# Kernel optimization log

Hardware: AMD Instinct MI355X
Metric: run time of the kernel (lower is better)

## Reference

```python
import jax, jax.numpy as jnp
import numpy as np

N, E, IN_DIM, OUT_DIM, R = 50000, 800000, 128, 128, 8


def setup_inputs() -> dict:
    key = jax.random.key(0)
    k1, k2, k3, k4, k5 = jax.random.split(key, 5)
    x = jax.random.normal(k1, (N, IN_DIM), dtype=jnp.float32)
    edge_index = jax.random.randint(k2, (2, E), 0, N, dtype=jnp.int32)
    edge_type = jax.random.randint(k3, (E,), 0, R, dtype=jnp.int32)
    # Xavier-uniform-ish init for parameters
    lim_w = float(np.sqrt(6.0 / (IN_DIM + OUT_DIM)))
    weight = jax.random.uniform(k4, (R, IN_DIM, OUT_DIM), dtype=jnp.float32, minval=-lim_w, maxval=lim_w)
    self_weight = jax.random.uniform(k5, (IN_DIM, OUT_DIM), dtype=jnp.float32, minval=-lim_w, maxval=lim_w)
    return {"x": x, "weight": weight, "self_weight": self_weight,
            "edge_index": edge_index, "edge_type": edge_type}


def reference(x, weight, self_weight, edge_index, edge_type):
    n = x.shape[0]
    r = weight.shape[0]
    d_out = weight.shape[2]
    src, dst = edge_index[0], edge_index[1]
    # undirected: symmetrize edges (directed=False)
    src_all = jnp.concatenate([src, dst])          # [2E]
    dst_all = jnp.concatenate([dst, src])          # [2E]
    et_all = jnp.concatenate([edge_type, edge_type])  # [2E]
    # transform all nodes by every relation weight once: [R, N, D_out]
    xw = jnp.einsum('ni,rio->rno', x, weight)
    # gather per-edge messages already transformed by their relation's W_r
    msg = xw[et_all, src_all]                      # [2E, D_out]
    # fused (relation, dst) segment id -> per-relation scatter-add
    seg = et_all.astype(jnp.int32) * n + dst_all
    agg = jax.ops.segment_sum(msg, seg, num_segments=r * n).reshape(r, n, d_out)
    deg = jax.ops.segment_sum(jnp.ones_like(seg, dtype=x.dtype), seg,
                              num_segments=r * n).reshape(r, n)
    deg_inv = jnp.where(deg > 0, 1.0 / jnp.maximum(deg, 1.0), jnp.zeros_like(deg))
    out = jnp.sum(agg * deg_inv[..., None], axis=0)  # [N, D_out]
    out = out + x @ self_weight                       # self-loop
    return out
```

## Files before the change

kernel.cpp:

```cpp
#include <hip/hip_runtime.h>

#define NN 50000
#define EE 800000
#define RR 8
#define DD 128
#define SS (NN*RR)
#define TE (2*EE)
#define NB 782
#define NBLK 391
#define NS (NB*NBLK)

typedef __attribute__((ext_vector_type(8))) short bf16x8;
typedef __attribute__((ext_vector_type(4))) float f32x4;

__device__ __forceinline__ unsigned short f2bf(float f){
  unsigned int u = __float_as_uint(f);
  u += 0x7fffu + ((u >> 16) & 1u);
  return (unsigned short)(u >> 16);
}
__device__ __forceinline__ float bf_lo(unsigned int w){ return __uint_as_float(w << 16); }
__device__ __forceinline__ float bf_hi(unsigned int w){ return __uint_as_float(w & 0xffff0000u); }

__device__ __forceinline__ void acc8(float* a, uint4 u){
  a[0] += bf_lo(u.x); a[1] += bf_hi(u.x);
  a[2] += bf_lo(u.y); a[3] += bf_hi(u.y);
  a[4] += bf_lo(u.z); a[5] += bf_hi(u.z);
  a[6] += bf_lo(u.w); a[7] += bf_hi(u.w);
}
__device__ __forceinline__ unsigned int pack2(float a, float b){
  return ((unsigned int)f2bf(b) << 16) | (unsigned int)f2bf(a);
}

__device__ __forceinline__ void dir_edge(const int* ei, const int* et, int j,
                                         int& s, int& d, int& t){
  if (j < EE){ s = ei[j]; d = ei[EE + j]; t = et[j]; }
  else { int jj = j - EE; s = ei[EE + jj]; d = ei[jj]; t = et[jj]; }
}

__global__ __launch_bounds__(256) void k_hist(const int* __restrict__ ei,
                                              const int* __restrict__ et,
                                              int* __restrict__ hist){
  __shared__ int h[NB];
  int tid = threadIdx.x, bid = blockIdx.x;
  for (int i = tid; i < NB; i += 256) h[i] = 0;
  __syncthreads();
  int j0 = bid*4096;
  for (int k = tid; k < 4096; k += 256){
    int j = j0 + k;
    if (j < TE){
      int s, d, t; dir_edge(ei, et, j, s, d, t);
      atomicAdd(&h[d >> 6], 1);
    }
  }
  __syncthreads();
  for (int i = tid; i < NB; i += 256) hist[i*NBLK + bid] = h[i];
}

__global__ __launch_bounds__(256) void k_scan1(int* __restrict__ hist,
                                               int* __restrict__ blksum){
  __shared__ int sd[256];
  int b = blockIdx.x, tid = threadIdx.x;
  int base = b*1024 + tid*4;
  int v0 = (base+0 < NS) ? hist[base+0] : 0;
  int v1 = (base+1 < NS) ? hist[base+1] : 0;
  int v2 = (base+2 < NS) ? hist[base+2] : 0;
  int v3 = (base+3 < NS) ? hist[base+3] : 0;
  int ts = v0+v1+v2+v3;
  sd[tid] = ts; __syncthreads();
  for (int o = 1; o < 256; o <<= 1){
    int t = (tid >= o) ? sd[tid-o] : 0;
    __syncthreads();
    sd[tid] += t;
    __syncthreads();
  }
  int ex = sd[tid] - ts;
  if (base+0 < NS) hist[base+0] = ex; ex += v0;
  if (base+1 < NS) hist[base+1] = ex; ex += v1;
  if (base+2 < NS) hist[base+2] = ex; ex += v2;
  if (base+3 < NS) hist[base+3] = ex;
  if (tid == 255) blksum[b] = sd[255];
}

__global__ __launch_bounds__(512) void k_scan2(int* __restrict__ blksum, int nb){
  __shared__ int sd[512];
  int tid = threadIdx.x;
  int v = (tid < nb) ? blksum[tid] : 0;
  sd[tid] = v; __syncthreads();
  for (int o = 1; o < 512; o <<= 1){
    int t = (tid >= o) ? sd[tid-o] : 0;
    __syncthreads();
    sd[tid] += t;
    __syncthreads();
  }
  if (tid < nb) blksum[tid] = sd[tid] - v;
}

__global__ __launch_bounds__(256) void k_scan3(int* __restrict__ hist,
                                               const int* __restrict__ blksum){
  int i = blockIdx.x*blockDim.x + threadIdx.x;
  if (i < NS) hist[i] += blksum[i >> 10];
}

__global__ __launch_bounds__(256) void k_part(const int* __restrict__ ei,
                                              const int* __restrict__ et,
                                              const int* __restrict__ S,
                                              unsigned int* __restrict__ P){
  __shared__ int cur[NB];
  int tid = threadIdx.x, bid = blockIdx.x;
  for (int i = tid; i < NB; i += 256) cur[i] = S[i*NBLK + bid];
  __syncthreads();
  int j0 = bid*4096;
  for (int k = tid; k < 4096; k += 256){
    int j = j0 + k;
    if (j < TE){
      int s, d, t; dir_edge(ei, et, j, s, d, t);
      int b = d >> 6;
      int p = atomicAdd(&cur[b], 1);
      P[p] = (unsigned int)s | ((unsigned int)(d & 63) << 17)
           | ((unsigned int)t << 23);
    }
  }
}

__global__ __launch_bounds__(256) void k_build(const unsigned int* __restrict__ P,
                                               const int* __restrict__ S,
                                               int* __restrict__ esrc,
                                               int* __restrict__ offs){
  __shared__ int h[512], cu[512], sd[256];
  int tid = threadIdx.x, b = blockIdx.x;
  int pstart = S[b*NBLK];
  int pend   = (b+1 < NB) ? S[(b+1)*NBLK] : TE;
  int ne = pend - pstart;
  h[2*tid] = 0; h[2*tid+1] = 0;
  __syncthreads();
  for (int k = tid; k < ne; k += 256){
    unsigned int u = P[pstart + k];
    int lseg = (int)(((u >> 17) & 63u)*8u + (u >> 23));
    atomicAdd(&h[lseg], 1);
  }
  __syncthreads();
  int v0 = h[2*tid], v1 = h[2*tid+1];
  int ts = v0 + v1;
  sd[tid] = ts; __syncthreads();
  for (int o = 1; o < 256; o <<= 1){
    int t = (tid >= o) ? sd[tid-o] : 0;
    __syncthreads();
    sd[tid] += t;
    __syncthreads();
  }
  int ex = sd[tid] - ts;
  cu[2*tid]   = pstart + ex;
  cu[2*tid+1] = pstart + ex + v0;
  int seg0 = b*512;
  if (seg0 + 2*tid     < SS) offs[seg0 + 2*tid]     = cu[2*tid];
  if (seg0 + 2*tid + 1 < SS) offs[seg0 + 2*tid + 1] = cu[2*tid+1];
  if (b == NB-1 && tid == 0) offs[SS] = TE;
  __syncthreads();
  for (int k = tid; k < ne; k += 256){
    unsigned int u = P[pstart + k];
    int lseg = (int)(((u >> 17) & 63u)*8u + (u >> 23));
    int r = atomicAdd(&cu[lseg], 1);
    esrc[r] = (int)(u & 0x1ffffu);
  }
}

__global__ __launch_bounds__(256) void k_conv(const float* __restrict__ x,
                                              const float* __restrict__ w,
                                              const float* __restrict__ sw,
                                              unsigned short* __restrict__ xb,
                                              unsigned short* __restrict__ wb){
  int i = blockIdx.x*blockDim.x + threadIdx.x;
  const int M1 = NN*DD/4;
  if (i < M1){
    float4 v = ((const float4*)x)[i];
    ushort4 o;
    o.x = f2bf(v.x); o.y = f2bf(v.y); o.z = f2bf(v.z); o.w = f2bf(v.w);
    ((ushort4*)xb)[i] = o;
  } else {
    int j = i - M1;
    if (j < 9*DD*DD){
      int r = j >> 14; int rem = j & 16383; int n = rem >> 7; int k = rem & 127;
      float v = (r < 8) ? w[r*16384 + k*128 + n] : sw[k*128 + n];
      wb[j] = f2bf(v);
    }
  }
}

__device__ __forceinline__ void issue4(const unsigned short* __restrict__ xb,
                                       int idxw, int gb, int gl,
                                       int ebase, int n, uint4 (&u)[4]){
  #pragma unroll
  for (int e = 0; e < 4; ++e){
    u[e] = make_uint4(0u,0u,0u,0u);
    if (e < n){
      int s = __shfl(idxw, gb + ebase + e);
      u[e] = *(const uint4*)(xb + (size_t)s*DD + gl*8);
    }
  }
}

__global__ __launch_bounds__(256, 2) void k_fused(
    const unsigned short* __restrict__ xb,
    const unsigned short* __restrict__ wb,
    const int* __restrict__ offs,
    const int* __restrict__ esrc,
    float* __restrict__ out)
{
  __shared__ __align__(16) unsigned short A[32][1160];
  const int tid  = threadIdx.x;
  const int wave = tid >> 6, lane = tid & 63;
  const int l15  = lane & 15, quad = lane >> 4;
  const int gw   = quad;
  const int gl   = l15;
  const int gb   = gw << 4;
  const int rowbase = blockIdx.x * 32;
  const int rw0 = rowbase + 8*wave;

  #pragma unroll
  for (int p = 0; p < 2; ++p){
    int rowl = 8*wave + 2*gw + p;
    int gd = rowbase + rowl;
    uint4 u = make_uint4(0u,0u,0u,0u);
    if (gd < NN) u = *(const uint4*)(xb + (size_t)gd*DD + gl*8);
    *(uint4*)&A[rowl][8*128 + gl*8] = u;
  }

  int oidx = rw0*8 + lane;
  int c0i = (oidx     < SS) ? oidx     : SS;
  int c1i = (oidx + 1 < SS) ? oidx + 1 : SS;
  int voff = offs[c0i];
  int vend = offs[c1i];
  int vcnt = vend - voff;

  int idxv[16];
  #pragma unroll
  for (int i = 0; i < 16; ++i){
    int off = __shfl(voff, gb + i);
    int cnt = __shfl(vcnt, gb + i);
    idxv[i] = (gl < cnt) ? esrc[off + gl] : 0;
  }

  uint4 U0[2][4], U1[2][4];
  {
    int c0 = __shfl(vcnt, gb + 0); c0 = c0 < 4 ? c0 : 4;
    int c1 = __shfl(vcnt, gb + 1); c1 = c1 < 4 ? c1 : 4;
    issue4(xb, idxv[0], gb, gl, 0, c0, U0[0]);
    issue4(xb, idxv[1], gb, gl, 0, c1, U1[0]);
  }

  #pragma unroll
  for (int ii = 0; ii < 16; ii += 2){
    const int cur = (ii >> 1) & 1;
    const int nxt = cur ^ 1;
    if (ii + 2 < 16){
      int c0 = __shfl(vcnt, gb + ii + 2); c0 = c0 < 4 ? c0 : 4;
      int c1 = __shfl(vcnt, gb + ii + 3); c1 = c1 < 4 ? c1 : 4;
      issue4(xb, idxv[ii+2], gb, gl, 0, c0, U0[nxt]);
      issue4(xb, idxv[ii+3], gb, gl, 0, c1, U1[nxt]);
    }
    int cnt0 = __shfl(vcnt, gb + ii),     cnt1 = __shfl(vcnt, gb + ii + 1);
    int off0 = __shfl(voff, gb + ii),     off1 = __shfl(voff, gb + ii + 1);
    int cm0  = cnt0 < 16 ? cnt0 : 16,     cm1  = cnt1 < 16 ? cnt1 : 16;
    float a0[8] = {0.f,0.f,0.f,0.f,0.f,0.f,0.f,0.f};
    float a1[8] = {0.f,0.f,0.f,0.f,0.f,0.f,0.f,0.f};
    #pragma unroll
    for (int e = 0; e < 4; ++e){ acc8(a0, U0[cur][e]); acc8(a1, U1[cur][e]); }
    int e0 = cm0 < 4 ? cm0 : 4, e1 = cm1 < 4 ? cm1 : 4;
    while (e0 < cm0 || e1 < cm1){
      int n0 = cm0 - e0; n0 = n0 < 0 ? 0 : (n0 > 4 ? 4 : n0);
      int n1 = cm1 - e1; n1 = n1 < 0 ? 0 : (n1 > 4 ? 4 : n1);
      uint4 t0[4], t1[4];
      issue4(xb, idxv[ii],   gb, gl, e0, n0, t0);
      issue4(xb, idxv[ii+1], gb, gl, e1, n1, t1);
      #pragma unroll
      for (int e = 0; e < 4; ++e){ acc8(a0, t0[e]); acc8(a1, t1[e]); }
      e0 += n0; e1 += n1;
    }
    if (cnt0 > 16){
      for (int e2 = 16; e2 < cnt0; ++e2){
        int s = esrc[off0 + e2];
        uint4 u = *(const uint4*)(xb + (size_t)s*DD + gl*8);
        acc8(a0, u);
      }
    }
    if (cnt1 > 16){
      for (int e2 = 16; e2 < cnt1; ++e2){
        int s = esrc[off1 + e2];
        uint4 u = *(const uint4*)(xb + (size_t)s*DD + gl*8);
        acc8(a1, u);
      }
    }
    float s0 = cnt0 > 0 ? 1.0f/(float)cnt0 : 0.f;
    float s1 = cnt1 > 0 ? 1.0f/(float)cnt1 : 0.f;
    int rowl = 8*wave + 2*gw + (ii >> 3);
    uint4 w0, w1;
    w0.x = pack2(a0[0]*s0, a0[1]*s0);
    w0.y = pack2(a0[2]*s0, a0[3]*s0);
    w0.z = pack2(a0[4]*s0, a0[5]*s0);
    w0.w = pack2(a0[6]*s0, a0[7]*s0);
    w1.x = pack2(a1[0]*s1, a1[1]*s1);
    w1.y = pack2(a1[2]*s1, a1[3]*s1);
    w1.z = pack2(a1[4]*s1, a1[5]*s1);
    w1.w = pack2(a1[6]*s1, a1[7]*s1);
    *(uint4*)&A[rowl][((ii    ) & 7)*128 + gl*8] = w0;
    *(uint4*)&A[rowl][((ii + 1) & 7)*128 + gl*8] = w1;
  }

  __syncthreads();

  f32x4 C[2][2];
  #pragma unroll
  for (int m = 0; m < 2; ++m){ C[m][0] = (f32x4)(0.f); C[m][1] = (f32x4)(0.f); }

  #pragma unroll
  for (int rr = 0; rr < 9; ++rr){
    const unsigned short* wr = wb + rr * 16384;
    bf16x8 bfrag[2][4];
    #pragma unroll
    for (int nt = 0; nt < 2; ++nt)
      #pragma unroll
      for (int ks = 0; ks < 4; ++ks)
        bfrag[nt][ks] = *(const bf16x8*)(wr + (wave*32 + nt*16 + l15)*128 + ks*32 + quad*8);
    #pragma unroll
    for (int m = 0; m < 2; ++m){
      #pragma unroll
      for (int ks = 0; ks < 4; ++ks){
        bf16x8 af = *(const bf16x8*)&A[m*16 + l15][rr*128 + ks*32 + quad*8];
        C[m][0] = __builtin_amdgcn_mfma_f32_16x16x32_bf16(af, bfrag[0][ks], C[m][0], 0, 0, 0);
        C[m][1] = __builtin_amdgcn_mfma_f32_16x16x32_bf16(af, bfrag[1][ks], C[m][1], 0, 0, 0);
      }
    }
  }

  #pragma unroll
  for (int m = 0; m < 2; ++m){
    #pragma unroll
    for (int nt = 0; nt < 2; ++nt){
      #pragma unroll
      for (int i = 0; i < 4; ++i){
        int row = m*16 + quad*4 + i;
        int gd  = rowbase + row;
        int col = wave*32 + nt*16 + l15;
        if (gd < NN) out[gd*DD + col] = C[m][nt][i];
      }
    }
  }
}

extern "C" void kernel_launch(void* const* d_in, const int* in_sizes, int n_in,
                              void* d_out, int out_size, void* d_ws, size_t ws_size,
                              hipStream_t stream){
  const float* x  = (const float*)d_in[0];
  const float* w  = (const float*)d_in[1];
  const float* sw = (const float*)d_in[2];
  const int*   ei = (const int*)d_in[3];
  const int*   et = (const int*)d_in[4];
  float* out = (float*)d_out;
  char* ws = (char*)d_ws;

  if (ws_size < (size_t)21100000) return;

  unsigned short* xb = (unsigned short*)(ws + 0);
  int*          hist = (int*)(ws + 0);
  int*        blksum = (int*)(ws + 1223168);
  unsigned int*    P = (unsigned int*)(ws + 1225216);
  int*          esrc = (int*)(ws + 12800000);
  int*          offs = (int*)(ws + 19200000);
  unsigned short* wb = (unsigned short*)(ws + 20800016);

  k_hist <<<NBLK, 256, 0, stream>>>(ei, et, hist);
  k_scan1<<<(NS + 1023)/1024, 256, 0, stream>>>(hist, blksum);
  k_scan2<<<1, 512, 0, stream>>>(blksum, (NS + 1023)/1024);
  k_scan3<<<(NS + 255)/256, 256, 0, stream>>>(hist, blksum);
  k_part <<<NBLK, 256, 0, stream>>>(ei, et, hist, P);
  k_build<<<NB, 256, 0, stream>>>(P, hist, esrc, offs);
  k_conv <<<(NN*DD/4 + 9*DD*DD + 255)/256, 256, 0, stream>>>(x, w, sw, xb, wb);
  k_fused<<<(NN + 31)/32, 256, 0, stream>>>(xb, wb, offs, esrc, out);
}
```

Measured before the change: 279.5 us.

## Shrink fused tile to 16 rows per block for higher occupancy

Each fused block now handles 16 destination nodes instead of 32. Each 16-lane group aggregates one node's 8 relation segments rather than two nodes' worth, so LDS per block halves and the launch bound rises to 4 blocks per SM. The self-loop A-operand is read straight from global xb inside the MFMA loop instead of being staged in LDS. The trade-off is twice as many blocks, each reloading the full 9 weight matrices, and the bounds checks are dropped because NN divides evenly by 16.

```diff
diff --git a/kernel.cpp b/kernel.cpp
--- a/kernel.cpp
+++ b/kernel.cpp
@@ -187,79 +187,71 @@
 }
 
 __device__ __forceinline__ void issue4(const unsigned short* __restrict__ xb,
-                                       int idxw, int gb, int gl,
+                                       int idxw, int lb, int gl,
                                        int ebase, int n, uint4 (&u)[4]){
   #pragma unroll
   for (int e = 0; e < 4; ++e){
     u[e] = make_uint4(0u,0u,0u,0u);
     if (e < n){
-      int s = __shfl(idxw, gb + ebase + e);
+      int s = __shfl(idxw, lb + ebase + e);
       u[e] = *(const uint4*)(xb + (size_t)s*DD + gl*8);
     }
   }
 }
 
-__global__ __launch_bounds__(256, 2) void k_fused(
+__global__ __launch_bounds__(256, 4) void k_fused(
     const unsigned short* __restrict__ xb,
     const unsigned short* __restrict__ wb,
     const int* __restrict__ offs,
     const int* __restrict__ esrc,
     float* __restrict__ out)
 {
-  __shared__ __align__(16) unsigned short A[32][1160];
+  __shared__ __align__(16) unsigned short A[16][1032];
   const int tid  = threadIdx.x;
   const int wave = tid >> 6, lane = tid & 63;
   const int l15  = lane & 15, quad = lane >> 4;
-  const int gw   = quad;
+  const int g    = quad;
   const int gl   = l15;
-  const int gb   = gw << 4;
-  const int rowbase = blockIdx.x * 32;
-  const int rw0 = rowbase + 8*wave;
-
-  #pragma unroll
-  for (int p = 0; p < 2; ++p){
-    int rowl = 8*wave + 2*gw + p;
-    int gd = rowbase + rowl;
-    uint4 u = make_uint4(0u,0u,0u,0u);
-    if (gd < NN) u = *(const uint4*)(xb + (size_t)gd*DD + gl*8);
-    *(uint4*)&A[rowl][8*128 + gl*8] = u;
-  }
-
-  int oidx = rw0*8 + lane;
-  int c0i = (oidx     < SS) ? oidx     : SS;
-  int c1i = (oidx + 1 < SS) ? oidx + 1 : SS;
-  int voff = offs[c0i];
-  int vend = offs[c1i];
-  int vcnt = vend - voff;
-
-  int idxv[16];
-  #pragma unroll
-  for (int i = 0; i < 16; ++i){
-    int off = __shfl(voff, gb + i);
-    int cnt = __shfl(vcnt, gb + i);
+  const int sb   = g << 3;
+  const int lb   = g << 4;
+  const int rowbase = blockIdx.x * 16;
+  const int rowl = 4*wave + g;
+
+  int voff = 0, vcnt = 0;
+  if (lane < 32){
+    int oidx = (rowbase + 4*wave)*8 + lane;
+    voff = offs[oidx];
+    vcnt = offs[oidx + 1] - voff;
+  }
+
+  int idxv[8];
+  #pragma unroll
+  for (int i = 0; i < 8; ++i){
+    int off = __shfl(voff, sb + i);
+    int cnt = __shfl(vcnt, sb + i);
     idxv[i] = (gl < cnt) ? esrc[off + gl] : 0;
   }
 
   uint4 U0[2][4], U1[2][4];
   {
-    int c0 = __shfl(vcnt, gb + 0); c0 = c0 < 4 ? c0 : 4;
-    int c1 = __shfl(vcnt, gb + 1); c1 = c1 < 4 ? c1 : 4;
-    issue4(xb, idxv[0], gb, gl, 0, c0, U0[0]);
-    issue4(xb, idxv[1], gb, gl, 0, c1, U1[0]);
-  }
-
-  #pragma unroll
-  for (int ii = 0; ii < 16; ii += 2){
+    int c0 = __shfl(vcnt, sb + 0); c0 = c0 < 4 ? c0 : 4;
+    int c1 = __shfl(vcnt, sb + 1); c1 = c1 < 4 ? c1 : 4;
+    issue4(xb, idxv[0], lb, gl, 0, c0, U0[0]);
+    issue4(xb, idxv[1], lb, gl, 0, c1, U1[0]);
+  }
+
+  #pragma unroll
+  for (int ii = 0; ii < 8; ii += 2){
     const int cur = (ii >> 1) & 1;
     const int nxt = cur ^ 1;
-    if (ii + 2 < 16){
-      int c0 = __shfl(vcnt, gb + ii + 2); c0 = c0 < 4 ? c0 : 4;
-      int c1 = __shfl(vcnt, gb + ii + 3); c1 = c1 < 4 ? c1 : 4;
-      issue4(xb, idxv[ii+2], gb, gl, 0, c0, U0[nxt]);
-      issue4(xb, idxv[ii+3], gb, gl, 0, c1, U1[nxt]);
-    }
-    int cnt0 = __shfl(vcnt, gb + ii),     cnt1 = __shfl(vcnt, gb + ii + 1);
-    int off0 = __shfl(voff, gb + ii),     off1 = __shfl(voff, gb + ii + 1);
+    if (ii + 2 < 8){
+      int c0 = __shfl(vcnt, sb + ii + 2); c0 = c0 < 4 ? c0 : 4;
+      int c1 = __shfl(vcnt, sb + ii + 3); c1 = c1 < 4 ? c1 : 4;
+      issue4(xb, idxv[ii+2], lb, gl, 0, c0, U0[nxt]);
+      issue4(xb, idxv[ii+3], lb, gl, 0, c1, U1[nxt]);
+    }
+    int cnt0 = __shfl(vcnt, sb + ii),     cnt1 = __shfl(vcnt, sb + ii + 1);
+    int off0 = __shfl(voff, sb + ii),     off1 = __shfl(voff, sb + ii + 1);
     int cm0  = cnt0 < 16 ? cnt0 : 16,     cm1  = cnt1 < 16 ? cnt1 : 16;
     float a0[8] = {0.f,0.f,0.f,0.f,0.f,0.f,0.f,0.f};
     float a1[8] = {0.f,0.f,0.f,0.f,0.f,0.f,0.f,0.f};
@@ -270,8 +262,8 @@
       int n0 = cm0 - e0; n0 = n0 < 0 ? 0 : (n0 > 4 ? 4 : n0);
       int n1 = cm1 - e1; n1 = n1 < 0 ? 0 : (n1 > 4 ? 4 : n1);
       uint4 t0[4], t1[4];
-      issue4(xb, idxv[ii],   gb, gl, e0, n0, t0);
-      issue4(xb, idxv[ii+1], gb, gl, e1, n1, t1);
+      issue4(xb, idxv[ii],   lb, gl, e0, n0, t0);
+      issue4(xb, idxv[ii+1], lb, gl, e1, n1, t1);
       #pragma unroll
       for (int e = 0; e < 4; ++e){ acc8(a0, t0[e]); acc8(a1, t1[e]); }
       e0 += n0; e1 += n1;
@@ -292,7 +284,6 @@
     }
     float s0 = cnt0 > 0 ? 1.0f/(float)cnt0 : 0.f;
     float s1 = cnt1 > 0 ? 1.0f/(float)cnt1 : 0.f;
-    int rowl = 8*wave + 2*gw + (ii >> 3);
     uint4 w0, w1;
     w0.x = pack2(a0[0]*s0, a0[1]*s0);
     w0.y = pack2(a0[2]*s0, a0[3]*s0);
@@ -302,15 +293,14 @@
     w1.y = pack2(a1[2]*s1, a1[3]*s1);
     w1.z = pack2(a1[4]*s1, a1[5]*s1);
     w1.w = pack2(a1[6]*s1, a1[7]*s1);
-    *(uint4*)&A[rowl][((ii    ) & 7)*128 + gl*8] = w0;
-    *(uint4*)&A[rowl][((ii + 1) & 7)*128 + gl*8] = w1;
-  }
-
-  __syncthreads();
-
-  f32x4 C[2][2];
-  #pragma unroll
-  for (int m = 0; m < 2; ++m){ C[m][0] = (f32x4)(0.f); C[m][1] = (f32x4)(0.f); }
+    *(uint4*)&A[rowl][(ii    )*128 + gl*8] = w0;
+    *(uint4*)&A[rowl][(ii + 1)*128 + gl*8] = w1;
+  }
+
+  __syncthreads();
+
+  f32x4 C[2];
+  C[0] = (f32x4)(0.f); C[1] = (f32x4)(0.f);
 
   #pragma unroll
   for (int rr = 0; rr < 9; ++rr){
@@ -322,27 +312,22 @@
       for (int ks = 0; ks < 4; ++ks)
         bfrag[nt][ks] = *(const bf16x8*)(wr + (wave*32 + nt*16 + l15)*128 + ks*32 + quad*8);
     #pragma unroll
-    for (int m = 0; m < 2; ++m){
-      #pragma unroll
-      for (int ks = 0; ks < 4; ++ks){
-        bf16x8 af = *(const bf16x8*)&A[m*16 + l15][rr*128 + ks*32 + quad*8];
-        C[m][0] = __builtin_amdgcn_mfma_f32_16x16x32_bf16(af, bfrag[0][ks], C[m][0], 0, 0, 0);
-        C[m][1] = __builtin_amdgcn_mfma_f32_16x16x32_bf16(af, bfrag[1][ks], C[m][1], 0, 0, 0);
-      }
-    }
-  }
-
-  #pragma unroll
-  for (int m = 0; m < 2; ++m){
+    for (int ks = 0; ks < 4; ++ks){
+      bf16x8 af;
+      if (rr < 8) af = *(const bf16x8*)&A[l15][rr*128 + ks*32 + quad*8];
+      else        af = *(const bf16x8*)(xb + (size_t)(rowbase + l15)*DD + ks*32 + quad*8);
+      C[0] = __builtin_amdgcn_mfma_f32_16x16x32_bf16(af, bfrag[0][ks], C[0], 0, 0, 0);
+      C[1] = __builtin_amdgcn_mfma_f32_16x16x32_bf16(af, bfrag[1][ks], C[1], 0, 0, 0);
+    }
+  }
+
+  #pragma unroll
+  for (int nt = 0; nt < 2; ++nt){
     #pragma unroll
-    for (int nt = 0; nt < 2; ++nt){
-      #pragma unroll
-      for (int i = 0; i < 4; ++i){
-        int row = m*16 + quad*4 + i;
-        int gd  = rowbase + row;
-        int col = wave*32 + nt*16 + l15;
-        if (gd < NN) out[gd*DD + col] = C[m][nt][i];
-      }
+    for (int i = 0; i < 4; ++i){
+      int row = quad*4 + i;
+      int col = wave*32 + nt*16 + l15;
+      out[(size_t)(rowbase + row)*DD + col] = C[nt][i];
     }
   }
 }
@@ -375,5 +360,5 @@
   k_part <<<NBLK, 256, 0, stream>>>(ei, et, hist, P);
   k_build<<<NB, 256, 0, stream>>>(P, hist, esrc, offs);
   k_conv <<<(NN*DD/4 + 9*DD*DD + 255)/256, 256, 0, stream>>>(x, w, sw, xb, wb);
-  k_fused<<<(NN + 31)/32, 256, 0, stream>>>(xb, wb, offs, esrc, out);
-}
+  k_fused<<<NN/16, 256, 0, stream>>>(xb, wb, offs, esrc, out);
+}
```

Measured after the change: 327.2 us. 17.1% more time.
